# Performance work log

Hardware: AMD Instinct MI355X
Metric: run time of the kernel (lower is better)

Reference implementation:

```python
import jax, jax.numpy as jnp
from jax import lax
import numpy as np

QMIN, QMAX = -127.0, 127.0
STRIDE = (1, 1)
PADDING = ((1, 1), (1, 1))
DILATION = (1, 1)
DN = ('NCHW', 'OIHW', 'NCHW')


def _quantize_x(x, scale_x):
    # symmetric static per-tensor int8 quantization
    return jnp.clip(jnp.round(x / scale_x), QMIN, QMAX)


def _quantize_w(w):
    # symmetric dynamic per-output-channel int8 quantization
    scale_w = jnp.max(jnp.abs(w), axis=(1, 2, 3), keepdims=True) / QMAX  # [O,1,1,1]
    q_w = jnp.clip(jnp.round(w / scale_w), QMIN, QMAX)
    return q_w, scale_w


def setup_inputs() -> dict:
    key = jax.random.key(0)
    kx, kw, kb = jax.random.split(key, 3)
    B, C, H, W = 32, 128, 56, 56
    O, kH, kW = 256, 3, 3
    x = jax.random.normal(kx, (B, C, H, W), jnp.float32)
    weight = jax.random.normal(kw, (O, C, kH, kW), jnp.float32) * 0.05
    bias = jax.random.normal(kb, (O,), jnp.float32)
    scale_x = jnp.asarray(0.02, jnp.float32)  # static per-tensor scale buffer
    # exact int8 product lookup table: lut[a+127, b+127] = a*b
    v = np.arange(-127, 128, dtype=np.int32)
    lut = jnp.asarray(v[:, None] * v[None, :])
    return {"x": x, "weight": weight, "bias": bias, "scale_x": scale_x, "lut": lut}


def reference(x, weight, bias, scale_x, lut):
    # lut holds the exact int8 product table, so bgemm_int8(q_x, q_w, lut) is an
    # exact integer GEMM; im2col + bGEMM == conv of quantized tensors.
    q_x = _quantize_x(x, scale_x)            # [B,C,H,W] integer-valued fp32
    q_w, scale_w = _quantize_w(weight)       # [O,C,kH,kW], [O,1,1,1]
    acc = lax.conv_general_dilated(
        q_x, q_w, STRIDE, PADDING, rhs_dilation=DILATION, dimension_numbers=DN
    )                                        # [B,O,OH,OW] integer-valued accumulator
    out = acc * scale_x * scale_w.reshape(1, -1, 1, 1)  # per-channel dequant
    return out + bias.reshape(1, -1, 1, 1)
```

## Files before the change

kernel.cpp:

```cpp
#include <hip/hip_runtime.h>


#define BATCH 32
#define CIN   128
#define HH    56
#define WW    56
#define OCH   256

typedef __attribute__((ext_vector_type(4))) int int4v;
typedef __attribute__((ext_vector_type(2))) long longx2;

#define QX_BYTES (32 * 56 * 56 * 128)
#define QW_BYTES (256 * 1152)
#define WS_NEEDED (QX_BYTES + QW_BYTES + 1024)

__device__ __forceinline__ void gload_lds16(const void* g, void* l) {
  __builtin_amdgcn_global_load_lds(
      (const __attribute__((address_space(1))) unsigned int*)g,
      (__attribute__((address_space(3))) unsigned int*)l, 16, 0, 0);
}

__global__ __launch_bounds__(256) void quant_w_kernel(
    const float* __restrict__ w, const float* __restrict__ sxp,
    char* __restrict__ qwf, float* __restrict__ alpha) {
  __shared__ float wf[1152];
  __shared__ float red[256];
  const int o = blockIdx.x;
  const int tid = threadIdx.x;
  const float* wrow = w + (size_t)o * 1152;
  float m = 0.f;
  for (int i = tid; i < 288; i += 256) {
    const float4 v = ((const float4*)wrow)[i];
    ((float4*)wf)[i] = v;
    m = fmaxf(m, fmaxf(fmaxf(fabsf(v.x), fabsf(v.y)),
                       fmaxf(fabsf(v.z), fabsf(v.w))));
  }
  red[tid] = m;
  __syncthreads();
  for (int s = 128; s > 0; s >>= 1) {
    if (tid < s) red[tid] = fmaxf(red[tid], red[tid + s]);
    __syncthreads();
  }
  const float sc = red[0] / 127.0f;
  if (tid == 0) alpha[o] = sc * sxp[0];
  if (tid < 36) {
    const int r = tid >> 2, c04 = tid & 3;
    const int og = o >> 5, t = (o >> 4) & 1, l16 = o & 15;
    unsigned int* base = (unsigned int*)(qwf + (size_t)og * 36864 +
                                         (size_t)(r * 4 + c04) * 1024);
#pragma unroll
    for (int quad = 0; quad < 4; ++quad) {
#pragma unroll
      for (int half = 0; half < 2; ++half) {
        unsigned int pk = 0;
#pragma unroll
        for (int k = 0; k < 4; ++k) {
          const int c = c04 * 32 + quad * 8 + half * 4 + k;
          const int q =
              (int)fminf(127.f, fmaxf(-127.f, rintf(wf[c * 9 + r] / sc)));
          pk |= ((unsigned int)(q & 255)) << (8 * k);
        }
        base[(l16 * 4 + quad) * 4 + t * 2 + half] = pk;
      }
    }
  }
}

__global__ __launch_bounds__(256) void quant_x_kernel(
    const float* __restrict__ x, const float* __restrict__ sxp,
    unsigned int* __restrict__ qxp) {
  __shared__ char ldsA[128 * 60];
  const int row = blockIdx.x;
  const int b = row / 56, h = row % 56;
  const float sx = sxp[0];
  for (int i = threadIdx.x; i < 1792; i += 256) {
    const int c = i / 14, f = i % 14;
    const float4 v =
        *(const float4*)(x + (((size_t)b * 128 + c) * 56 + h) * 56 + 4 * f);
    unsigned int pk;
    pk  = (unsigned int)((int)fminf(127.f, fmaxf(-127.f, rintf(v.x / sx))) & 255);
    pk |= ((unsigned int)((int)fminf(127.f, fmaxf(-127.f, rintf(v.y / sx))) & 255)) << 8;
    pk |= ((unsigned int)((int)fminf(127.f, fmaxf(-127.f, rintf(v.z / sx))) & 255)) << 16;
    pk |= ((unsigned int)((int)fminf(127.f, fmaxf(-127.f, rintf(v.w / sx))) & 255)) << 24;
    *(unsigned int*)(ldsA + c * 60 + 4 * f) = pk;
  }
  __syncthreads();
  unsigned int* orow = qxp + (size_t)row * 56 * 32;
  for (int i = threadIdx.x; i < 1792; i += 256) {
    const int w = i >> 5, jd = i & 31;
    const int c0 = (jd ^ (((w + 1) & 15) << 1)) << 2;
    unsigned int pk = 0;
#pragma unroll
    for (int k = 0; k < 4; ++k)
      pk |= ((unsigned int)(unsigned char)ldsA[(c0 + k) * 60 + w]) << (8 * k);
    orow[i] = pk;
  }
}

#define XSLAB 8448

__global__ __launch_bounds__(512, 4) void conv_kernel(
    const char* __restrict__ qxp, const char* __restrict__ qwf,
    const float* __restrict__ alpha, const float* __restrict__ bias,
    float* __restrict__ out) {
  __shared__ __attribute__((aligned(16))) char Xs8[3 * XSLAB];

  const int id = blockIdx.x;
  const int xcd = id & 7;
  const int bi = xcd * 224 + (id >> 3);
  const int b  = bi / 56;
  const int oh = bi % 56;
  const int tid = threadIdx.x;
  const int wave = tid >> 6, lane = tid & 63;
  const int l16 = lane & 15, quad = lane >> 4;

  const longx2* wb2 = (const longx2*)(qwf + (size_t)wave * 36864) +
                      (l16 * 4 + quad);
  longx2 ap[2][4];
#pragma unroll
  for (int c04 = 0; c04 < 4; ++c04) ap[0][c04] = wb2[(size_t)c04 * 64];

  for (int kh = 0; kh < 3; ++kh) {
    const int ih = oh - 1 + kh;
    char* slab = Xs8 + kh * XSLAB;
    if (ih >= 0 && ih < HH) {
      const char* src = qxp + ((size_t)b * 56 + ih) * 7168;
      if (tid < 448) gload_lds16(src + tid * 16, slab + 128 + tid * 16);
      for (int i = tid; i < 320; i += 512) {
        const int cg = i >> 5, dw = i & 31;
        const int col = (cg == 0) ? 0 : 56 + cg;
        ((unsigned int*)slab)[col * 32 + dw] = 0u;
      }
    } else {
      for (int i = tid; i < 2112; i += 512) ((unsigned int*)slab)[i] = 0u;
    }
  }

  int4v acc[2][4];
#pragma unroll
  for (int t = 0; t < 2; ++t)
#pragma unroll
    for (int u = 0; u < 4; ++u) acc[t][u] = (int4v){0, 0, 0, 0};

  __syncthreads();

  long bops[2][4];
  {
    const int ph0 = (l16 & 15) << 3;
    const int boff0 = (quad * 8) ^ ph0;
#pragma unroll
    for (int u = 0; u < 4; ++u)
      bops[0][u] = *(const long*)(Xs8 + (u * 16 + l16) * 128 + boff0);
  }
#pragma unroll
  for (int step = 0; step < 36; ++step) {
    const int g = step >> 2, c04 = step & 3;
    if (step + 1 < 36) {
      const int gn = (step + 1) >> 2, cn = (step + 1) & 3;
      const int khn = gn / 3, kwn = gn % 3;
      const char* Xkn = Xs8 + khn * XSLAB;
      const int phn = ((l16 + kwn) & 15) << 3;
      const int boffn = (cn * 32 + quad * 8) ^ phn;
#pragma unroll
      for (int u = 0; u < 4; ++u)
        bops[(step + 1) & 1][u] =
            *(const long*)(Xkn + (u * 16 + l16 + kwn) * 128 + boffn);
    }
    if (c04 == 0 && g < 8) {
#pragma unroll
      for (int cc = 0; cc < 4; ++cc)
        ap[(g + 1) & 1][cc] = wb2[(size_t)((g + 1) * 4 + cc) * 64];
    }
#pragma unroll
    for (int u = 0; u < 4; ++u) {
      acc[0][u] = __builtin_amdgcn_mfma_i32_16x16x32_i8(
          ap[g & 1][c04][0], bops[step & 1][u], acc[0][u], 0, 0, 0);
      acc[1][u] = __builtin_amdgcn_mfma_i32_16x16x32_i8(
          ap[g & 1][c04][1], bops[step & 1][u], acc[1][u], 0, 0, 0);
    }
  }

#pragma unroll
  for (int t = 0; t < 2; ++t) {
#pragma unroll
    for (int r = 0; r < 4; ++r) {
      const int o = wave * 32 + t * 16 + quad * 4 + r;
      const float al = alpha[o], bz = bias[o];
      float* orow = out + (((size_t)b * OCH + o) * HH + oh) * WW;
#pragma unroll
      for (int u = 0; u < 4; ++u) {
        const int ow = u * 16 + l16;
        if (ow < WW) orow[ow] = (float)acc[t][u][r] * al + bz;
      }
    }
  }
}

#define FAS_ROW 392
#define FXS_ROW 136
#define FLDS_XS (128 * FAS_ROW)
#define FLDS_SC (FLDS_XS + 66 * FXS_ROW)
#define FLDS_AL (FLDS_SC + 512)
#define FLDS_BI (FLDS_AL + 512)
#define FLDS_RED (FLDS_BI + 512)
#define FLDS_TOT (FLDS_RED + 1024)

__global__ __launch_bounds__(256) void conv_fused_kernel(
    const float* __restrict__ x, const float* __restrict__ w,
    const float* __restrict__ bias, const float* __restrict__ sxp,
    float* __restrict__ out) {
  __shared__ __attribute__((aligned(16))) char lds[FLDS_TOT];
  char* As8 = lds;
  char* Xs8 = lds + FLDS_XS;
  float* scaleS = (float*)(lds + FLDS_SC);
  float* alphaS = (float*)(lds + FLDS_AL);
  float* biasS  = (float*)(lds + FLDS_BI);
  float* red    = (float*)(lds + FLDS_RED);

  const int bi = blockIdx.x;
  const int b  = bi / 56;
  const int oh = bi % 56;
  const int o0 = blockIdx.y * 128;
  const int tid = threadIdx.x;
  const int wave = tid >> 6, lane = tid & 63;
  const int l16 = lane & 15, quad = lane >> 4;
  const float sx = sxp[0];

  int m_r[4], n_r[4];
  {
    int4v zz = {0, 0, 0, 0};
    long a1 = 0, b1 = 0, a2 = 0, b2 = 0;
    if (quad == 0) { a1 = 1L; b1 = (long)(l16 + 1); a2 = (long)(l16 + 1); b2 = 1L; }
    int4v d1 = __builtin_amdgcn_mfma_i32_16x16x32_i8(a1, b1, zz, 0, 0, 0);
    int4v d2 = __builtin_amdgcn_mfma_i32_16x16x32_i8(a2, b2, zz, 0, 0, 0);
#pragma unroll
    for (int r = 0; r < 4; ++r) { n_r[r] = (d1[r] - 1) & 15; m_r[r] = (d2[r] - 1) & 15; }
  }
  {
    const int o = tid >> 1, half = tid & 1;
    const float4* p = (const float4*)(w + (size_t)(o0 + o) * 1152 + half * 576);
    float m = 0.f;
#pragma unroll 4
    for (int i = 0; i < 144; ++i) {
      const float4 v = p[i];
      m = fmaxf(m, fmaxf(fmaxf(fabsf(v.x), fabsf(v.y)), fmaxf(fabsf(v.z), fabsf(v.w))));
    }
    red[tid] = m;
  }
  __syncthreads();
  {
    const int o = tid >> 1;
    if ((tid & 1) == 0) {
      const float sc = fmaxf(red[2 * o], red[2 * o + 1]) / 127.0f;
      scaleS[o] = sc; alphaS[o] = sc * sx; biasS[o] = bias[o0 + o];
    }
  }
  int4v acc[2][4];
#pragma unroll
  for (int t = 0; t < 2; ++t)
#pragma unroll
    for (int u = 0; u < 4; ++u) acc[t][u] = (int4v){0, 0, 0, 0};

  for (int kh = 0; kh < 3; ++kh) {
    const int ih = oh - 1 + kh;
    const bool row_ok = (ih >= 0) && (ih < HH);
    __syncthreads();
    for (int idx = tid; idx < 66 * 128; idx += 256) {
      const int col = idx % 66, c = idx / 66, iw = col - 1;
      int q = 0;
      if (row_ok && iw >= 0 && iw < WW) {
        const float xv = x[(((size_t)b * CIN + c) * HH + ih) * WW + iw];
        q = (int)fminf(127.f, fmaxf(-127.f, rintf(xv / sx)));
      }
      Xs8[col * FXS_ROW + c] = (char)q;
    }
    for (int idx = tid; idx < 16384; idx += 256) {
      const int c = idx & 127, o = idx >> 7;
      const float s = scaleS[o];
      const float* wp = w + (size_t)(o0 + o) * 1152 + c * 9 + kh * 3;
#pragma unroll
      for (int kw = 0; kw < 3; ++kw) {
        const int q = (int)fminf(127.f, fmaxf(-127.f, rintf(wp[kw] / s)));
        As8[o * FAS_ROW + kw * 128 + c] = (char)q;
      }
    }
    __syncthreads();
    const int obase = wave * 32;
#pragma unroll
    for (int kw = 0; kw < 3; ++kw) {
#pragma unroll
      for (int c0 = 0; c0 < 128; c0 += 32) {
        long aop[2], bop[4];
#pragma unroll
        for (int t = 0; t < 2; ++t)
          aop[t] = *(const long*)(As8 + (obase + t * 16 + l16) * FAS_ROW + kw * 128 + c0 + quad * 8);
#pragma unroll
        for (int u = 0; u < 4; ++u)
          bop[u] = *(const long*)(Xs8 + (u * 16 + l16 + kw) * FXS_ROW + c0 + quad * 8);
#pragma unroll
        for (int t = 0; t < 2; ++t)
#pragma unroll
          for (int u = 0; u < 4; ++u)
            acc[t][u] = __builtin_amdgcn_mfma_i32_16x16x32_i8(aop[t], bop[u], acc[t][u], 0, 0, 0);
      }
    }
  }
#pragma unroll
  for (int t = 0; t < 2; ++t) {
#pragma unroll
    for (int u = 0; u < 4; ++u) {
#pragma unroll
      for (int r = 0; r < 4; ++r) {
        const int ol = wave * 32 + t * 16 + m_r[r];
        const int ow = u * 16 + n_r[r];
        if (ow < WW)
          out[(((size_t)b * OCH + o0 + ol) * HH + oh) * WW + ow] =
              (float)acc[t][u][r] * alphaS[ol] + biasS[ol];
      }
    }
  }
}

extern "C" void kernel_launch(void* const* d_in, const int* in_sizes, int n_in,
                              void* d_out, int out_size, void* d_ws, size_t ws_size,
                              hipStream_t stream) {
  const float *x = nullptr, *w = nullptr, *bias = nullptr, *sx = nullptr;
  for (int i = 0; i < n_in; ++i) {
    const int s = in_sizes[i];
    if (s == BATCH * CIN * HH * WW) x = (const float*)d_in[i];
    else if (s == OCH * CIN * 9)    w = (const float*)d_in[i];
    else if (s == OCH)              bias = (const float*)d_in[i];
    else if (s == 1)                sx = (const float*)d_in[i];
  }
  if (!x || !w || !bias || !sx) {
    x = (const float*)d_in[0]; w = (const float*)d_in[1];
    bias = (const float*)d_in[2]; sx = (const float*)d_in[3];
  }
  float* out = (float*)d_out;

  if (ws_size >= (size_t)WS_NEEDED) {
    unsigned int* qxp = (unsigned int*)d_ws;
    char* qwf = (char*)d_ws + QX_BYTES;
    float* alpha = (float*)((char*)d_ws + QX_BYTES + QW_BYTES);
    quant_w_kernel<<<OCH, 256, 0, stream>>>(w, sx, qwf, alpha);
    quant_x_kernel<<<BATCH * HH, 256, 0, stream>>>(x, sx, qxp);
    conv_kernel<<<BATCH * HH, 512, 0, stream>>>(
        (const char*)qxp, qwf, alpha, bias, out);
  } else {
    conv_fused_kernel<<<dim3(BATCH * HH, 2), 256, 0, stream>>>(x, w, bias, sx, out);
  }
}
```

Before: 189.7 us.

## Switch conv to 16x16x64 int8 MFMA and split output channels across blocks

Replaces the 16x16x32 int8 MFMA with the double-K 16x16x64 variant, so each step consumes 16-byte operands, halving the number of MFMA issues and LDS reads per K. The weight packing and the activation LDS swizzle are re-laid out to match the 16-byte-per-lane operand format. Each block now handles 128 output channels with 256 threads, and the grid is doubled, which improves scheduling granularity. The cost is that each input slab is loaded twice, once per channel half.

Result: faster. 185.2 us (-2.4%).

```diff
diff --git a/kernel.cpp b/kernel.cpp
--- a/kernel.cpp
+++ b/kernel.cpp
@@ -8,7 +8,6 @@
 #define OCH   256
 
 typedef __attribute__((ext_vector_type(4))) int int4v;
-typedef __attribute__((ext_vector_type(2))) long longx2;
 
 #define QX_BYTES (32 * 56 * 56 * 128)
 #define QW_BYTES (256 * 1152)
@@ -43,26 +42,24 @@
   }
   const float sc = red[0] / 127.0f;
   if (tid == 0) alpha[o] = sc * sxp[0];
-  if (tid < 36) {
-    const int r = tid >> 2, c04 = tid & 3;
+  if (tid < 72) {
+    const int r = tid >> 3, c02 = (tid >> 2) & 1, quad = tid & 3;
     const int og = o >> 5, t = (o >> 4) & 1, l16 = o & 15;
-    unsigned int* base = (unsigned int*)(qwf + (size_t)og * 36864 +
-                                         (size_t)(r * 4 + c04) * 1024);
-#pragma unroll
-    for (int quad = 0; quad < 4; ++quad) {
-#pragma unroll
-      for (int half = 0; half < 2; ++half) {
-        unsigned int pk = 0;
-#pragma unroll
-        for (int k = 0; k < 4; ++k) {
-          const int c = c04 * 32 + quad * 8 + half * 4 + k;
-          const int q =
-              (int)fminf(127.f, fmaxf(-127.f, rintf(wf[c * 9 + r] / sc)));
-          pk |= ((unsigned int)(q & 255)) << (8 * k);
-        }
-        base[(l16 * 4 + quad) * 4 + t * 2 + half] = pk;
-      }
-    }
+    int4v pk;
+#pragma unroll
+    for (int d = 0; d < 4; ++d) {
+      unsigned int p = 0;
+#pragma unroll
+      for (int k = 0; k < 4; ++k) {
+        const int c = c02 * 64 + quad * 16 + d * 4 + k;
+        const int q =
+            (int)fminf(127.f, fmaxf(-127.f, rintf(wf[c * 9 + r] / sc)));
+        p |= ((unsigned int)(q & 255)) << (8 * k);
+      }
+      pk[d] = (int)p;
+    }
+    *(int4v*)(qwf + (size_t)og * 36864 + ((r * 2 + c02) * 2 + t) * 1024 +
+              (quad * 16 + l16) * 16) = pk;
   }
 }
 
@@ -88,7 +85,7 @@
   unsigned int* orow = qxp + (size_t)row * 56 * 32;
   for (int i = threadIdx.x; i < 1792; i += 256) {
     const int w = i >> 5, jd = i & 31;
-    const int c0 = (jd ^ (((w + 1) & 15) << 1)) << 2;
+    const int c0 = (jd ^ (((w + 1) & 7) << 2)) << 2;
     unsigned int pk = 0;
 #pragma unroll
     for (int k = 0; k < 4; ++k)
@@ -99,7 +96,7 @@
 
 #define XSLAB 8448
 
-__global__ __launch_bounds__(512, 4) void conv_kernel(
+__global__ __launch_bounds__(256, 4) void conv_kernel(
     const char* __restrict__ qxp, const char* __restrict__ qwf,
     const float* __restrict__ alpha, const float* __restrict__ bias,
     float* __restrict__ out) {
@@ -107,32 +104,40 @@
 
   const int id = blockIdx.x;
   const int xcd = id & 7;
-  const int bi = xcd * 224 + (id >> 3);
+  int kk = id >> 3;
+  const int yy = (kk >= 224) ? 1 : 0;
+  kk -= yy * 224;
+  const int bi = xcd * 224 + kk;
   const int b  = bi / 56;
   const int oh = bi % 56;
+  const int o0 = yy * 128;
   const int tid = threadIdx.x;
   const int wave = tid >> 6, lane = tid & 63;
   const int l16 = lane & 15, quad = lane >> 4;
 
-  const longx2* wb2 = (const longx2*)(qwf + (size_t)wave * 36864) +
-                      (l16 * 4 + quad);
-  longx2 ap[2][4];
-#pragma unroll
-  for (int c04 = 0; c04 < 4; ++c04) ap[0][c04] = wb2[(size_t)c04 * 64];
+  const int4v* wbA =
+      (const int4v*)(qwf + (size_t)(yy * 4 + wave) * 36864) + lane;
+  int4v ap[2][2][2];
+#pragma unroll
+  for (int c02 = 0; c02 < 2; ++c02)
+#pragma unroll
+    for (int t = 0; t < 2; ++t)
+      ap[0][c02][t] = wbA[(size_t)(c02 * 2 + t) * 64];
 
   for (int kh = 0; kh < 3; ++kh) {
     const int ih = oh - 1 + kh;
     char* slab = Xs8 + kh * XSLAB;
     if (ih >= 0 && ih < HH) {
       const char* src = qxp + ((size_t)b * 56 + ih) * 7168;
-      if (tid < 448) gload_lds16(src + tid * 16, slab + 128 + tid * 16);
-      for (int i = tid; i < 320; i += 512) {
+      for (int i = tid; i < 448; i += 256)
+        gload_lds16(src + i * 16, slab + 128 + i * 16);
+      for (int i = tid; i < 320; i += 256) {
         const int cg = i >> 5, dw = i & 31;
         const int col = (cg == 0) ? 0 : 56 + cg;
         ((unsigned int*)slab)[col * 32 + dw] = 0u;
       }
     } else {
-      for (int i = tid; i < 2112; i += 512) ((unsigned int*)slab)[i] = 0u;
+      for (int i = tid; i < 2112; i += 256) ((unsigned int*)slab)[i] = 0u;
     }
   }
 
@@ -144,39 +149,42 @@
 
   __syncthreads();
 
-  long bops[2][4];
+  int4v bops[2][4];
   {
-    const int ph0 = (l16 & 15) << 3;
-    const int boff0 = (quad * 8) ^ ph0;
+    const int ph0 = (l16 & 7) << 4;
+    const int boff0 = (quad * 16) ^ ph0;
 #pragma unroll
     for (int u = 0; u < 4; ++u)
-      bops[0][u] = *(const long*)(Xs8 + (u * 16 + l16) * 128 + boff0);
-  }
-#pragma unroll
-  for (int step = 0; step < 36; ++step) {
-    const int g = step >> 2, c04 = step & 3;
-    if (step + 1 < 36) {
-      const int gn = (step + 1) >> 2, cn = (step + 1) & 3;
+      bops[0][u] = *(const int4v*)(Xs8 + (u * 16 + l16) * 128 + boff0);
+  }
+#pragma unroll
+  for (int ss = 0; ss < 18; ++ss) {
+    const int g = ss >> 1, c02 = ss & 1;
+    if (ss + 1 < 18) {
+      const int gn = (ss + 1) >> 1, cn = (ss + 1) & 1;
       const int khn = gn / 3, kwn = gn % 3;
       const char* Xkn = Xs8 + khn * XSLAB;
-      const int phn = ((l16 + kwn) & 15) << 3;
-      const int boffn = (cn * 32 + quad * 8) ^ phn;
+      const int phn = ((l16 + kwn) & 7) << 4;
+      const int boffn = (cn * 64 + quad * 16) ^ phn;
 #pragma unroll
       for (int u = 0; u < 4; ++u)
-        bops[(step + 1) & 1][u] =
-            *(const long*)(Xkn + (u * 16 + l16 + kwn) * 128 + boffn);
-    }
-    if (c04 == 0 && g < 8) {
-#pragma unroll
-      for (int cc = 0; cc < 4; ++cc)
-        ap[(g + 1) & 1][cc] = wb2[(size_t)((g + 1) * 4 + cc) * 64];
+        bops[(ss + 1) & 1][u] =
+            *(const int4v*)(Xkn + (u * 16 + l16 + kwn) * 128 + boffn);
+    }
+    if (c02 == 0 && g < 8) {
+#pragma unroll
+      for (int cc = 0; cc < 2; ++cc)
+#pragma unroll
+        for (int t = 0; t < 2; ++t)
+          ap[(g + 1) & 1][cc][t] =
+              wbA[(size_t)(((g + 1) * 2 + cc) * 2 + t) * 64];
     }
 #pragma unroll
     for (int u = 0; u < 4; ++u) {
-      acc[0][u] = __builtin_amdgcn_mfma_i32_16x16x32_i8(
-          ap[g & 1][c04][0], bops[step & 1][u], acc[0][u], 0, 0, 0);
-      acc[1][u] = __builtin_amdgcn_mfma_i32_16x16x32_i8(
-          ap[g & 1][c04][1], bops[step & 1][u], acc[1][u], 0, 0, 0);
+      acc[0][u] = __builtin_amdgcn_mfma_i32_16x16x64_i8(
+          ap[g & 1][c02][0], bops[ss & 1][u], acc[0][u], 0, 0, 0);
+      acc[1][u] = __builtin_amdgcn_mfma_i32_16x16x64_i8(
+          ap[g & 1][c02][1], bops[ss & 1][u], acc[1][u], 0, 0, 0);
     }
   }
 
@@ -184,7 +192,7 @@
   for (int t = 0; t < 2; ++t) {
 #pragma unroll
     for (int r = 0; r < 4; ++r) {
-      const int o = wave * 32 + t * 16 + quad * 4 + r;
+      const int o = o0 + wave * 32 + t * 16 + quad * 4 + r;
       const float al = alpha[o], bz = bias[o];
       float* orow = out + (((size_t)b * OCH + o) * HH + oh) * WW;
 #pragma unroll
@@ -226,13 +234,14 @@
   const int l16 = lane & 15, quad = lane >> 4;
   const float sx = sxp[0];
 
+  typedef __attribute__((ext_vector_type(4))) int int4vf;
   int m_r[4], n_r[4];
   {
-    int4v zz = {0, 0, 0, 0};
+    int4vf zz = {0, 0, 0, 0};
     long a1 = 0, b1 = 0, a2 = 0, b2 = 0;
     if (quad == 0) { a1 = 1L; b1 = (long)(l16 + 1); a2 = (long)(l16 + 1); b2 = 1L; }
-    int4v d1 = __builtin_amdgcn_mfma_i32_16x16x32_i8(a1, b1, zz, 0, 0, 0);
-    int4v d2 = __builtin_amdgcn_mfma_i32_16x16x32_i8(a2, b2, zz, 0, 0, 0);
+    int4vf d1 = __builtin_amdgcn_mfma_i32_16x16x32_i8(a1, b1, zz, 0, 0, 0);
+    int4vf d2 = __builtin_amdgcn_mfma_i32_16x16x32_i8(a2, b2, zz, 0, 0, 0);
 #pragma unroll
     for (int r = 0; r < 4; ++r) { n_r[r] = (d1[r] - 1) & 15; m_r[r] = (d2[r] - 1) & 15; }
   }
@@ -255,11 +264,11 @@
       scaleS[o] = sc; alphaS[o] = sc * sx; biasS[o] = bias[o0 + o];
     }
   }
-  int4v acc[2][4];
+  int4vf acc[2][4];
 #pragma unroll
   for (int t = 0; t < 2; ++t)
 #pragma unroll
-    for (int u = 0; u < 4; ++u) acc[t][u] = (int4v){0, 0, 0, 0};
+    for (int u = 0; u < 4; ++u) acc[t][u] = (int4vf){0, 0, 0, 0};
 
   for (int kh = 0; kh < 3; ++kh) {
     const int ih = oh - 1 + kh;
@@ -344,7 +353,7 @@
     float* alpha = (float*)((char*)d_ws + QX_BYTES + QW_BYTES);
     quant_w_kernel<<<OCH, 256, 0, stream>>>(w, sx, qwf, alpha);
     quant_x_kernel<<<BATCH * HH, 256, 0, stream>>>(x, sx, qxp);
-    conv_kernel<<<BATCH * HH, 512, 0, stream>>>(
+    conv_kernel<<<BATCH * HH * 2, 256, 0, stream>>>(
         (const char*)qxp, qwf, alpha, bias, out);
   } else {
     conv_fused_kernel<<<dim3(BATCH * HH, 2), 256, 0, stream>>>(x, w, bias, sx, out);
```
